# Kernel tuning notes

Measured on AMD Instinct MI355X. Metric: run time of the kernel, lower is better.

Reference implementation:

```python
import jax, jax.numpy as jnp
import numpy as np

D_MODEL = 1024
N_HEADS = 16
HEAD_DIM = D_MODEL // N_HEADS


def setup_inputs() -> dict:
    key = jax.random.key(0)
    k1, k2, k3 = jax.random.split(key, 3)
    x = jax.random.normal(k1, (4, 2048, D_MODEL), dtype=jnp.float32)
    # torch Linear weight is [out, in]; y = x @ W.T
    w_qkv = jax.random.normal(k2, (3 * D_MODEL, D_MODEL), dtype=jnp.float32) * (1.0 / np.sqrt(D_MODEL))
    w_proj = jax.random.normal(k3, (D_MODEL, D_MODEL), dtype=jnp.float32) * (1.0 / np.sqrt(D_MODEL))
    return {"x": x, "w_qkv": w_qkv, "w_proj": w_proj}


def reference(x, w_qkv, w_proj):
    B, T, C = x.shape
    qkv = jnp.einsum('btc,oc->bto', x, w_qkv)  # [B,T,3C]
    q, k, v = jnp.split(qkv, 3, axis=-1)
    # [B,T,H,D] -> [B,H,T,D]
    def to_heads(t):
        return t.reshape(B, T, N_HEADS, HEAD_DIM).transpose(0, 2, 1, 3)
    q, k, v = to_heads(q), to_heads(k), to_heads(v)
    scale = 1.0 / np.sqrt(HEAD_DIM).astype(np.float32)
    scores = jnp.einsum('bhqd,bhkd->bhqk', q, k) * scale  # [B,H,T,T]
    causal = jnp.tril(jnp.ones((T, T), dtype=bool))
    scores = jnp.where(causal, scores, jnp.finfo(scores.dtype).min)
    attn = jax.nn.softmax(scores, axis=-1)
    out = jnp.einsum('bhqk,bhkd->bhqd', attn, v)  # [B,H,T,D]
    out = out.transpose(0, 2, 1, 3).reshape(B, T, C)
    return jnp.einsum('btc,oc->bto', out, w_proj)
```

## Files before the change

### kernel.cpp

```cpp
#include <hip/hip_runtime.h>

#define B_ 4
#define T_ 2048
#define C_ 1024
#define H_ 16
#define D_ 64

typedef __bf16 bf16;
typedef bf16 bf16x8 __attribute__((ext_vector_type(8)));
typedef bf16 bf16x4v __attribute__((ext_vector_type(4)));
typedef float f32x4 __attribute__((ext_vector_type(4)));

__device__ __forceinline__ int probe_is_f32(const void* p, int lane) {
  float v = fminf(fabsf((float)((const bf16*)p)[lane]), 100.f);
#pragma unroll
  for (int o = 1; o < 64; o <<= 1) v += __shfl_xor(v, o, 64);
  return v > 300.f ? 1 : 0;
}

__device__ __forceinline__ void gload16(const void* g, void* l) {
  __builtin_amdgcn_global_load_lds(
      (const __attribute__((address_space(1))) void*)g,
      (__attribute__((address_space(3))) void*)l, 16, 0, 0);
}

__global__ __launch_bounds__(256) void cvt_bf16(const void* __restrict__ src,
                                                size_t elofs,
                                                bf16* __restrict__ dst,
                                                int n8) {
  if (!probe_is_f32(src, threadIdx.x & 63)) return;
  int i = blockIdx.x * 256 + threadIdx.x;
  if (i >= n8) return;
  const float* s = (const float*)src + elofs + (size_t)i * 8;
  f32x4 u0 = *(const f32x4*)s;
  f32x4 u1 = *(const f32x4*)(s + 4);
  bf16x8 o;
#pragma unroll
  for (int j = 0; j < 4; ++j) { o[j] = (bf16)u0[j]; o[4 + j] = (bf16)u1[j]; }
  *(bf16x8*)(dst + (size_t)i * 8) = o;
}

__global__ __launch_bounds__(256) void transpose_o(const bf16* __restrict__ src,
                                                   bf16* __restrict__ dst) {
  int i = blockIdx.x * 256 + threadIdx.x;
  int d8 = i & 7;
  int r = i >> 3;
  int t = r & (T_ - 1);
  int r2 = r >> 11;
  int h = r2 & (H_ - 1);
  int b = r2 >> 4;
  bf16x8 v =
      *(const bf16x8*)(src + ((size_t)(b * H_ + h) * T_ + t) * D_ + d8 * 8);
  *(bf16x8*)(dst + ((size_t)(b * T_ + t) * C_) + h * D_ + d8 * 8) = v;
}

__global__ __launch_bounds__(256, 3) void gemm_bt(
    const void* __restrict__ A, const bf16* __restrict__ Ab, int arowbase,
    int tmofs, const void* __restrict__ W, const bf16* __restrict__ Wcvt,
    int M, int N, int K, int amode, int omode, void* __restrict__ out,
    bf16* __restrict__ qb, bf16* __restrict__ kb, bf16* __restrict__ vtb,
    const void* __restrict__ px, const void* __restrict__ pwq,
    const void* __restrict__ pwp, int bsel) {
  __shared__ __align__(16) char lds[16384];
  char* ldsA = lds;
  char* ldsB = lds + 8192;

  const int ntiles = N >> 7;
  int bid = blockIdx.x;
  if ((gridDim.x & 7) == 0) {
    int cpx = gridDim.x >> 3;
    bid = (bid & 7) * cpx + (bid >> 3);
  }
  const int tm = tmofs + bid / ntiles;
  const int tn = bid % ntiles;
  const int tid = threadIdx.x;
  const int lane = tid & 63;
  const int wv = tid >> 6;
  const int wm = wv >> 1, wn = wv & 1;
  const int lm = lane & 15, lq = lane >> 4;

  const int fx = probe_is_f32(px, lane);
  const int fwq = probe_is_f32(pwq, lane);
  const int fwp = probe_is_f32(pwp, lane);
  const int outF32 = fx | fwq | fwp;
  const int bF32 = bsel ? fwp : fwq;
  const bf16* Wb = bF32 ? Wcvt : (const bf16*)W;
  const bf16* Asrc = (amode == 0 && fx) ? Ab : (const bf16*)A;
  const int rowadj = (amode == 0 && fx) ? arowbase : 0;

  size_t boff[2], aoffb[2];
#pragma unroll
  for (int h = 0; h < 2; ++h) {
    int c = tid + h * 256, rbk = c >> 6, ll = c & 63;
    boff[h] = (size_t)(tn * 128 + rbk * 16 + (ll & 15)) * K + (ll >> 4) * 8;
    aoffb[h] =
        (size_t)(tm * 128 + rbk * 16 + (ll & 15) - rowadj) * K + (ll >> 4) * 8;
  }

  f32x4 acc[4][4] = {};

  for (int k0 = 0; k0 < K; k0 += 32) {
    __syncthreads();
#pragma unroll
    for (int h = 0; h < 2; ++h) {
      gload16(Asrc + aoffb[h] + k0, ldsA + (tid + h * 256) * 16);
      gload16(Wb + boff[h] + k0, ldsB + (tid + h * 256) * 16);
    }
    __syncthreads();

    bf16x8 af[4], bff[4];
#pragma unroll
    for (int i = 0; i < 4; ++i)
      af[i] = *(const bf16x8*)(ldsA + (wm * 4 + i) * 1024 + lane * 16);
#pragma unroll
    for (int j = 0; j < 4; ++j)
      bff[j] = *(const bf16x8*)(ldsB + (wn * 4 + j) * 1024 + lane * 16);
#pragma unroll
    for (int i = 0; i < 4; ++i)
#pragma unroll
      for (int j = 0; j < 4; ++j)
        acc[i][j] = __builtin_amdgcn_mfma_f32_16x16x32_bf16(af[i], bff[j],
                                                            acc[i][j], 0, 0, 0);
  }

  if (omode == 0) {
#pragma unroll
    for (int i = 0; i < 4; ++i) {
      int row0 = tm * 128 + wm * 64 + i * 16 + lq * 4;
#pragma unroll
      for (int j = 0; j < 4; ++j) {
        int col = tn * 128 + wn * 64 + j * 16 + lm;
#pragma unroll
        for (int r = 0; r < 4; ++r) {
          size_t idx = (size_t)(row0 + r) * N + col;
          if (outF32) ((float*)out)[idx] = acc[i][j][r];
          else        ((bf16*)out)[idx]  = (bf16)acc[i][j][r];
        }
      }
    }
  } else {
#pragma unroll
    for (int j = 0; j < 4; ++j) {
      int o = tn * 128 + wn * 64 + j * 16 + lm;
      int which = o >> 10;
      int c = o & 1023;
      int h = c >> 6, d = c & 63;
#pragma unroll
      for (int i = 0; i < 4; ++i) {
        int row0 = tm * 128 + wm * 64 + i * 16 + lq * 4;
        int b = row0 >> 11, t0 = row0 & 2047;
        if (which == 2) {
          bf16x4v pk;
#pragma unroll
          for (int r = 0; r < 4; ++r) pk[r] = (bf16)acc[i][j][r];
          *(bf16x4v*)(vtb + ((size_t)((b * H_ + h) * D_ + d)) * T_ + t0) = pk;
        } else {
          bf16* dst = (which == 0) ? qb : kb;
#pragma unroll
          for (int r = 0; r < 4; ++r)
            dst[((size_t)((b * H_ + h) * T_ + t0 + r)) * D_ + d] =
                (bf16)acc[i][j][r];
        }
      }
    }
  }
}

__global__ __launch_bounds__(256, 4) void attn_fwd(bf16* __restrict__ Q,
                                                   const bf16* __restrict__ Kk,
                                                   const bf16* __restrict__ Vt) {
  __shared__ __align__(16) char lds[12288];
  char* ldsK = lds;
  char* ldsV = lds + 4096;
  char* ldsP = lds + 8192;

  const int tid = threadIdx.x;
  const int bh = blockIdx.x & 63;
  const int pi = blockIdx.x >> 6;
  const int lane = tid & 63;
  const int wv = tid >> 6;
  const int lm = lane & 15, lq = lane >> 4;

  const int kRow = (wv >> 1) * 16 + lm;
  const int kD = (wv & 1) * 32 + lq * 8;
  const int vD = wv * 16 + lm;

  const bf16* ksrc = Kk + ((size_t)(bh * T_ + kRow)) * D_ + kD;
  const bf16* vsrc = Vt + ((size_t)(bh * D_ + vD)) * T_ + lq * 8;
  char* myP = ldsP + wv * 1024;

  bf16x8 vones;
#pragma unroll
  for (int j = 0; j < 8; ++j) vones[j] = (bf16)1.0f;

#pragma unroll 1
  for (int phase = 0; phase < 2; ++phase) {
    const int qt = phase ? (31 - pi) : pi;
    const int q0w = qt * 64 + wv * 16;

    bf16x8 qa[2];
    {
      const bf16* qbase = Q + ((size_t)(bh * T_ + q0w + lm)) * D_ + lq * 8;
      qa[0] = *(const bf16x8*)(qbase);
      qa[1] = *(const bf16x8*)(qbase + 32);
    }

    f32x4 oacc[4] = {};
    f32x4 lacc = {};
    const int jend = qt * 64 + 64;

    for (int j0 = 0; j0 < jend; j0 += 32) {
      __syncthreads();
      gload16(ksrc + (size_t)j0 * D_, ldsK + tid * 16);
      gload16(vsrc + j0, ldsV + tid * 16);
      __syncthreads();

      bf16x8 kf[2][2], vf[4];
#pragma unroll
      for (int t = 0; t < 2; ++t)
#pragma unroll
        for (int kc = 0; kc < 2; ++kc)
          kf[t][kc] = *(const bf16x8*)(ldsK + (t * 2 + kc) * 1024 + lane * 16);
#pragma unroll
      for (int nt = 0; nt < 4; ++nt)
        vf[nt] = *(const bf16x8*)(ldsV + nt * 1024 + lane * 16);

#pragma unroll
      for (int t = 0; t < 2; ++t) {
        f32x4 s = {};
        __builtin_amdgcn_s_setprio(1);
        s = __builtin_amdgcn_mfma_f32_16x16x32_bf16(qa[0], kf[t][0], s, 0, 0, 0);
        s = __builtin_amdgcn_mfma_f32_16x16x32_bf16(qa[1], kf[t][1], s, 0, 0, 0);
        __builtin_amdgcn_s_setprio(0);
        int kcol = j0 + t * 16 + lm;
        int chunkc = t * 2 + (lm >> 3);
        int jj = lm & 7;
        char* pdst = myP + (chunkc * 16 + lq * 4) * 16 + jj * 2;
        if (j0 + t * 16 + 15 <= q0w) {
#pragma unroll
          for (int r = 0; r < 4; ++r) {
            bf16 pb = (bf16)__expf(s[r] * 0.125f);
            *(bf16*)(pdst + r * 16) = pb;
          }
        } else {
#pragma unroll
          for (int r = 0; r < 4; ++r) {
            int qrow = q0w + lq * 4 + r;
            float p = (kcol <= qrow) ? __expf(s[r] * 0.125f) : 0.0f;
            *(bf16*)(pdst + r * 16) = (bf16)p;
          }
        }
      }
      bf16x8 pf = *(const bf16x8*)(myP + lane * 16);
      __builtin_amdgcn_s_setprio(1);
      lacc = __builtin_amdgcn_mfma_f32_16x16x32_bf16(pf, vones, lacc, 0, 0, 0);
#pragma unroll
      for (int nt = 0; nt < 4; ++nt)
        oacc[nt] = __builtin_amdgcn_mfma_f32_16x16x32_bf16(pf, vf[nt], oacc[nt],
                                                            0, 0, 0);
      __builtin_amdgcn_s_setprio(0);
    }

    float rinv[4];
#pragma unroll
    for (int r = 0; r < 4; ++r) rinv[r] = 1.0f / fmaxf(lacc[r], 1e-30f);
#pragma unroll
    for (int nt = 0; nt < 4; ++nt)
#pragma unroll
      for (int r = 0; r < 4; ++r) {
        int t = q0w + lq * 4 + r;
        Q[((size_t)(bh * T_ + t)) * D_ + nt * 16 + lm] =
            (bf16)(oacc[nt][r] * rinv[r]);
      }
  }
}

extern "C" void kernel_launch(void* const* d_in, const int* in_sizes, int n_in,
                              void* d_out, int out_size, void* d_ws,
                              size_t ws_size, hipStream_t stream) {
  const void* x = d_in[0];
  const void* wqkv = d_in[1];
  const void* wproj = d_in[2];

  const size_t NE = (size_t)B_ * T_ * C_;
  bf16* qb = (bf16*)d_ws;
  bf16* kb = qb + NE;
  bf16* vtb = (bf16*)d_out;
  bf16* wqkvb = vtb + NE;
  bf16* xb1 = wqkvb + 3 * C_ * C_;
  bf16* ob = kb;
  bf16* wprojb = qb;

  const int M = B_ * T_;
  const int Mh = M / 2;
  const int nh8 = Mh * C_ / 8;

  cvt_bf16<<<(3 * C_ * C_ / 8) / 256, 256, 0, stream>>>(wqkv, 0, wqkvb,
                                                        3 * C_ * C_ / 8);
  cvt_bf16<<<nh8 / 256, 256, 0, stream>>>(x, 0, xb1, nh8);
  gemm_bt<<<(Mh / 128) * (3 * C_ / 128), 256, 0, stream>>>(
      x, xb1, 0, 0, wqkv, wqkvb, M, 3 * C_, C_,
      0, 1, nullptr, qb, kb, vtb, x, wqkv, wproj,
      0);
  cvt_bf16<<<nh8 / 256, 256, 0, stream>>>(x, (size_t)Mh * C_, xb1, nh8);
  gemm_bt<<<(Mh / 128) * (3 * C_ / 128), 256, 0, stream>>>(
      x, xb1, Mh, Mh / 128, wqkv, wqkvb, M, 3 * C_, C_,
      0, 1, nullptr, qb, kb, vtb, x, wqkv, wproj,
      0);
  attn_fwd<<<(T_ / 64 / 2) * B_ * H_, 256, 0, stream>>>(qb, kb, vtb);
  transpose_o<<<(int)(NE / 8 / 256), 256, 0, stream>>>(qb, ob);
  cvt_bf16<<<(C_ * C_ / 8) / 256, 256, 0, stream>>>(wproj, 0, wprojb,
                                                    C_ * C_ / 8);
  gemm_bt<<<(M / 128) * (C_ / 128), 256, 0, stream>>>(
      ob, ob, 0, 0, wproj, wprojb, M, C_, C_,
      0, 0, d_out, nullptr, nullptr, nullptr, x, wqkv,
      wproj, 1);
}
```

Baseline: 313.1 us.

## Split attention key range across two wave groups with LDS reduction

Doubles the attention block to 512 threads, with two groups of four waves each processing half of the causal key range for the same query tile. Partial output and row-sum accumulators are combined through LDS before normalization and write-back. This halves the serial key loop per wave and raises parallelism, at the cost of extra LDS, barriers and a reduction step. Priority hints around MFMA are also removed.

New measurement: 577.9 us. 84.6% more time.

```diff
diff --git a/kernel.cpp b/kernel.cpp
--- a/kernel.cpp
+++ b/kernel.cpp
@@ -166,28 +166,30 @@
   }
 }
 
-__global__ __launch_bounds__(256, 4) void attn_fwd(bf16* __restrict__ Q,
+__global__ __launch_bounds__(512, 8) void attn_fwd(bf16* __restrict__ Q,
                                                    const bf16* __restrict__ Kk,
                                                    const bf16* __restrict__ Vt) {
-  __shared__ __align__(16) char lds[12288];
-  char* ldsK = lds;
-  char* ldsV = lds + 4096;
-  char* ldsP = lds + 8192;
+  __shared__ __align__(16) char lds[24576];
 
   const int tid = threadIdx.x;
   const int bh = blockIdx.x & 63;
   const int pi = blockIdx.x >> 6;
   const int lane = tid & 63;
   const int wv = tid >> 6;
+  const int g = wv >> 2;
+  const int wvl = wv & 3;
   const int lm = lane & 15, lq = lane >> 4;
 
-  const int kRow = (wv >> 1) * 16 + lm;
-  const int kD = (wv & 1) * 32 + lq * 8;
-  const int vD = wv * 16 + lm;
+  const int kRow = (wvl >> 1) * 16 + lm;
+  const int kD = (wvl & 1) * 32 + lq * 8;
+  const int vD = wvl * 16 + lm;
 
   const bf16* ksrc = Kk + ((size_t)(bh * T_ + kRow)) * D_ + kD;
   const bf16* vsrc = Vt + ((size_t)(bh * D_ + vD)) * T_ + lq * 8;
-  char* myP = ldsP + wv * 1024;
+
+  char* ldsKg = lds + g * 8192;
+  char* ldsVg = ldsKg + 4096;
+  char* myP = lds + 16384 + wv * 1024;
 
   bf16x8 vones;
 #pragma unroll
@@ -196,7 +198,7 @@
 #pragma unroll 1
   for (int phase = 0; phase < 2; ++phase) {
     const int qt = phase ? (31 - pi) : pi;
-    const int q0w = qt * 64 + wv * 16;
+    const int q0w = qt * 64 + wvl * 16;
 
     bf16x8 qa[2];
     {
@@ -207,12 +209,15 @@
 
     f32x4 oacc[4] = {};
     f32x4 lacc = {};
-    const int jend = qt * 64 + 64;
-
-    for (int j0 = 0; j0 < jend; j0 += 32) {
+    const int nsteps = qt + 1;
+    const int jbase = g * nsteps * 32;
+
+#pragma unroll 1
+    for (int i = 0; i < nsteps; ++i) {
+      const int j0 = jbase + i * 32;
       __syncthreads();
-      gload16(ksrc + (size_t)j0 * D_, ldsK + tid * 16);
-      gload16(vsrc + j0, ldsV + tid * 16);
+      gload16(ksrc + (size_t)j0 * D_, ldsKg + wvl * 1024 + lane * 16);
+      gload16(vsrc + j0, ldsVg + wvl * 1024 + lane * 16);
       __syncthreads();
 
       bf16x8 kf[2][2], vf[4];
@@ -220,18 +225,16 @@
       for (int t = 0; t < 2; ++t)
 #pragma unroll
         for (int kc = 0; kc < 2; ++kc)
-          kf[t][kc] = *(const bf16x8*)(ldsK + (t * 2 + kc) * 1024 + lane * 16);
+          kf[t][kc] = *(const bf16x8*)(ldsKg + (t * 2 + kc) * 1024 + lane * 16);
 #pragma unroll
       for (int nt = 0; nt < 4; ++nt)
-        vf[nt] = *(const bf16x8*)(ldsV + nt * 1024 + lane * 16);
+        vf[nt] = *(const bf16x8*)(ldsVg + nt * 1024 + lane * 16);
 
 #pragma unroll
       for (int t = 0; t < 2; ++t) {
         f32x4 s = {};
-        __builtin_amdgcn_s_setprio(1);
         s = __builtin_amdgcn_mfma_f32_16x16x32_bf16(qa[0], kf[t][0], s, 0, 0, 0);
         s = __builtin_amdgcn_mfma_f32_16x16x32_bf16(qa[1], kf[t][1], s, 0, 0, 0);
-        __builtin_amdgcn_s_setprio(0);
         int kcol = j0 + t * 16 + lm;
         int chunkc = t * 2 + (lm >> 3);
         int jj = lm & 7;
@@ -252,26 +255,39 @@
         }
       }
       bf16x8 pf = *(const bf16x8*)(myP + lane * 16);
-      __builtin_amdgcn_s_setprio(1);
       lacc = __builtin_amdgcn_mfma_f32_16x16x32_bf16(pf, vones, lacc, 0, 0, 0);
 #pragma unroll
       for (int nt = 0; nt < 4; ++nt)
         oacc[nt] = __builtin_amdgcn_mfma_f32_16x16x32_bf16(pf, vf[nt], oacc[nt],
                                                             0, 0, 0);
-      __builtin_amdgcn_s_setprio(0);
-    }
-
-    float rinv[4];
-#pragma unroll
-    for (int r = 0; r < 4; ++r) rinv[r] = 1.0f / fmaxf(lacc[r], 1e-30f);
-#pragma unroll
-    for (int nt = 0; nt < 4; ++nt)
-#pragma unroll
-      for (int r = 0; r < 4; ++r) {
-        int t = q0w + lq * 4 + r;
-        Q[((size_t)(bh * T_ + t)) * D_ + nt * 16 + lm] =
-            (bf16)(oacc[nt][r] * rinv[r]);
-      }
+    }
+
+    __syncthreads();
+    if (g == 1) {
+      char* ox = lds + wvl * 4096 + lane * 64;
+#pragma unroll
+      for (int nt = 0; nt < 4; ++nt) *(f32x4*)(ox + nt * 16) = oacc[nt];
+      *(f32x4*)(lds + 16384 + wvl * 1024 + lane * 16) = lacc;
+    }
+    __syncthreads();
+    if (g == 0) {
+      char* ox = lds + wvl * 4096 + lane * 64;
+#pragma unroll
+      for (int nt = 0; nt < 4; ++nt)
+        oacc[nt] += *(const f32x4*)(ox + nt * 16);
+      lacc += *(const f32x4*)(lds + 16384 + wvl * 1024 + lane * 16);
+      float rinv[4];
+#pragma unroll
+      for (int r = 0; r < 4; ++r) rinv[r] = 1.0f / fmaxf(lacc[r], 1e-30f);
+#pragma unroll
+      for (int nt = 0; nt < 4; ++nt)
+#pragma unroll
+        for (int r = 0; r < 4; ++r) {
+          int t = q0w + lq * 4 + r;
+          Q[((size_t)(bh * T_ + t)) * D_ + nt * 16 + lm] =
+              (bf16)(oacc[nt][r] * rinv[r]);
+        }
+    }
   }
 }
 
@@ -307,7 +323,7 @@
       x, xb1, Mh, Mh / 128, wqkv, wqkvb, M, 3 * C_, C_,
       0, 1, nullptr, qb, kb, vtb, x, wqkv, wproj,
       0);
-  attn_fwd<<<(T_ / 64 / 2) * B_ * H_, 256, 0, stream>>>(qb, kb, vtb);
+  attn_fwd<<<(T_ / 64 / 2) * B_ * H_, 512, 0, stream>>>(qb, kb, vtb);
   transpose_o<<<(int)(NE / 8 / 256), 256, 0, stream>>>(qb, ob);
   cvt_bf16<<<(C_ * C_ / 8) / 256, 256, 0, stream>>>(wproj, 0, wprojb,
                                                     C_ * C_ / 8);
```
